# Optimization experiments

Measured on AMD Instinct MI355X. Metric: run time of the kernel, lower is better.

## Reference

```python
import jax, jax.numpy as jnp
import numpy as np

N_BLOCKS, N_LAYERS_PER, RADIX = 4, 10, 2
DILATIONS = [RADIX ** i for i in range(N_LAYERS_PER)] * N_BLOCKS  # 40 layers
NL = len(DILATIONS)
C = 256    # residual_channels
DC = 256   # dilation_channels
SC = 256   # skip_channels
AUX = 80
HOP = 256
CLASSES = 256


def _dilated_causal_conv(x, w, b, d):
    # x: [B, Cin, T], w: [Cout, Cin, K], causal left-pad d*(K-1) (zeropad=True path)
    pad = d * (w.shape[-1] - 1)
    out = jax.lax.conv_general_dilated(
        x, w, window_strides=(1,), padding=[(pad, 0)], rhs_dilation=(d,),
        dimension_numbers=('NCH', 'OIH', 'NCH'))
    return out + b[None, :, None]


def _linear_interp(c, scale):
    # F.interpolate(mode='linear', align_corners=False): out_len = in_len*scale
    Fr = c.shape[-1]
    T = Fr * scale
    pos = jnp.maximum((jnp.arange(T, dtype=jnp.float32) + 0.5) / scale - 0.5, 0.0)
    i0 = jnp.floor(pos).astype(jnp.int32)
    i1 = jnp.minimum(i0 + 1, Fr - 1)
    w = (pos - i0.astype(jnp.float32))
    return c[..., i0] * (1.0 - w) + c[..., i1] * w


def setup_inputs() -> dict:
    key = jax.random.key(0)
    ks = jax.random.split(key, 16)
    B, T, FR = 1, 4096, 16
    s = 0.05
    x = jax.random.randint(ks[0], (B, T), 0, CLASSES)
    y = jax.random.normal(ks[1], (B, AUX, FR), jnp.float32)
    emb_w = jax.random.normal(ks[2], (CLASSES, C), jnp.float32) * s
    emb_w = emb_w.at[CLASSES // 2 - 1].set(0.0)  # padding_idx row is zero
    cond_w = jax.random.normal(ks[3], (2 * DC * NL, AUX), jnp.float32) * s  # 1x1 conv, no bias
    layer_w = jax.random.normal(ks[4], (NL, 2 * DC, C, RADIX), jnp.float32) * s
    layer_b = jax.random.normal(ks[5], (NL, 2 * DC), jnp.float32) * s
    wo_w = jax.random.normal(ks[6], (NL - 1, C + SC, DC), jnp.float32) * s  # res+skip 1x1
    wo_b = jax.random.normal(ks[7], (NL - 1, C + SC), jnp.float32) * s
    last_wo_w = jax.random.normal(ks[8], (SC, DC), jnp.float32) * s         # last layer: skip only
    last_wo_b = jax.random.normal(ks[9], (SC,), jnp.float32) * s
    end1_w = jax.random.normal(ks[10], (SC, SC), jnp.float32) * s
    end1_b = jax.random.normal(ks[11], (SC,), jnp.float32) * s
    end2_w = jax.random.normal(ks[12], (CLASSES, SC), jnp.float32) * s
    end2_b = jax.random.normal(ks[13], (CLASSES,), jnp.float32) * s
    return dict(x=x, y=y, zeropad=1, emb_w=emb_w, cond_w=cond_w,
                layer_w=layer_w, layer_b=layer_b, wo_w=wo_w, wo_b=wo_b,
                last_wo_w=last_wo_w, last_wo_b=last_wo_b,
                end1_w=end1_w, end1_b=end1_b, end2_w=end2_w, end2_b=end2_b)


def reference(x, y, zeropad, emb_w, cond_w, layer_w, layer_b, wo_w, wo_b,
              last_wo_w, last_wo_b, end1_w, end1_b, end2_w, end2_b):
    # embedding + tanh -> [B, C, T]
    h = jnp.tanh(emb_w[x]).transpose(0, 2, 1)
    T = h.shape[-1]
    # conditioner (1x1 conv, no bias) then linear upsample by hop_length
    cond = jnp.einsum('oa,baf->bof', cond_w, y)          # [B, 2*DC*NL, FR]
    cond = _linear_interp(cond, HOP)[..., :T]            # [B, 2*DC*NL, T]
    skip_sum = jnp.zeros((h.shape[0], SC, T), h.dtype)
    for i, d in enumerate(DILATIONS):
        z = _dilated_causal_conv(h, layer_w[i], layer_b[i], d)
        z = z + cond[:, 2 * DC * i:2 * DC * (i + 1)]
        a, g = jnp.split(z, 2, axis=1)
        z = jnp.tanh(a) * jax.nn.sigmoid(g)              # gated activation
        if i < NL - 1:
            o = jnp.einsum('oc,bct->bot', wo_w[i], z) + wo_b[i][None, :, None]
            h = h + o[:, :C]                             # residual
            skip = o[:, C:]
        else:
            skip = jnp.einsum('oc,bct->bot', last_wo_w, z) + last_wo_b[None, :, None]
        skip_sum = skip_sum + skip
    out = jax.nn.relu(skip_sum)
    out = jnp.einsum('oc,bct->bot', end1_w, out) + end1_b[None, :, None]
    out = jax.nn.relu(out)
    out = jnp.einsum('oc,bct->bot', end2_w, out) + end2_b[None, :, None]
    return out  # [B, classes, T]
```

## Files before the change

kernel.cpp:

```cpp
#include <hip/hip_runtime.h>
#include <math.h>

#define T_LEN 4096

typedef __bf16 bf16x8 __attribute__((ext_vector_type(8)));
typedef float  f32x4  __attribute__((ext_vector_type(4)));

union U2 { __bf16 h[2]; unsigned int u; };
union U4 { __bf16 h[4]; uint2 u; };
union U8 { __bf16 h[8]; uint4 u; };

__device__ __forceinline__ void gll16(const void* g, void* l) {
    __builtin_amdgcn_global_load_lds(
        (const __attribute__((address_space(1))) void*)g,
        (__attribute__((address_space(3))) void*)l, 16, 0, 0);
}

__device__ __forceinline__ size_t bfidx(int t, int c) {
    return (size_t)(t >> 4) * 4096 + (size_t)((c >> 5) * 512)
         + (size_t)((((t & 15) + ((c >> 3) & 3) * 16)) * 8) + (c & 7);
}

__global__ __launch_bounds__(256) void embed_kernel(
    const int* __restrict__ x, const float* __restrict__ emb_w,
    float* __restrict__ h, __bf16* __restrict__ XF_hi, __bf16* __restrict__ XF_lo,
    float* __restrict__ skip)
{
    int idx = blockIdx.x * 256 + threadIdx.x;
    int t  = idx & 4095;
    int c2 = (idx >> 12) * 2;
    float2 v = *(const float2*)&emb_w[(size_t)x[t] * 256 + c2];
    float e0 = tanhf(v.x), e1 = tanhf(v.y);
    h[(size_t)c2 * T_LEN + t]       = e0;
    h[(size_t)(c2 + 1) * T_LEN + t] = e1;
    U2 ph, pl;
    ph.h[0] = (__bf16)e0; ph.h[1] = (__bf16)e1;
    pl.h[0] = (__bf16)(e0 - (float)ph.h[0]);
    pl.h[1] = (__bf16)(e1 - (float)ph.h[1]);
    size_t o = bfidx(t, c2);
    *(unsigned int*)(XF_hi + o) = ph.u;
    *(unsigned int*)(XF_lo + o) = pl.u;
    skip[idx * 2]     = 0.0f;
    skip[idx * 2 + 1] = 0.0f;
}

__global__ __launch_bounds__(256) void cond_kernel(
    const float* __restrict__ cond_w, const float* __restrict__ y,
    float* __restrict__ condf)
{
    int idx = blockIdx.x * 256 + threadIdx.x;
    if (idx < 20480 * 16) {
        int o = idx >> 4, f = idx & 15;
        float acc = 0.0f;
        for (int a = 0; a < 80; ++a)
            acc += cond_w[o * 80 + a] * y[a * 16 + f];
        condf[idx] = acc;
    }
}

__global__ __launch_bounds__(256) void skip_cvt_kernel(
    const float* __restrict__ skip,
    __bf16* __restrict__ SF_hi, __bf16* __restrict__ SF_lo)
{
    int idx = blockIdx.x * 256 + threadIdx.x;
    int t  = idx & 4095;
    int c2 = (idx >> 12) * 2;
    float s0 = fmaxf(skip[(size_t)c2 * T_LEN + t], 0.0f);
    float s1 = fmaxf(skip[(size_t)(c2 + 1) * T_LEN + t], 0.0f);
    U2 ph, pl;
    ph.h[0] = (__bf16)s0; ph.h[1] = (__bf16)s1;
    pl.h[0] = (__bf16)(s0 - (float)ph.h[0]);
    pl.h[1] = (__bf16)(s1 - (float)ph.h[1]);
    size_t o = bfidx(t, c2);
    *(unsigned int*)(SF_hi + o) = ph.u;
    *(unsigned int*)(SF_lo + o) = pl.u;
}

__global__ __launch_bounds__(256) void cvt_conv_kernel(
    const float* __restrict__ lw, __bf16* __restrict__ dst)
{
    int f = blockIdx.x * 256 + threadIdx.x;
    int lane = f & 63;
    int mi   = (f >> 6) & 3;
    int kc   = (f >> 8) & 15;
    int gb   = f >> 12;
    int lr = lane & 15, lg = lane >> 4;
    int by = gb & 7, L = gb >> 3;
    int row  = by * 64 + mi * 16 + lr;
    int grow = (row & 1) ? 256 + (row >> 1) : (row >> 1);
    int tap  = (kc >= 8) ? 1 : 0;
    int cb   = (kc & 7) * 32 + lg * 8;
    const float* src = lw + (size_t)L * 262144 + (size_t)grow * 512 + 2 * cb + tap;
    U8 hi, lo;
    #pragma unroll
    for (int j = 0; j < 8; ++j) {
        float v = src[2 * j];
        __bf16 h = (__bf16)v;
        hi.h[j] = h;
        lo.h[j] = (__bf16)(v - (float)h);
    }
    size_t base = (size_t)(gb * 16 + kc) * 4096;
    *(uint4*)(dst + base + (size_t)mi * 512 + lane * 8)        = hi.u;
    *(uint4*)(dst + base + 2048 + (size_t)mi * 512 + lane * 8) = lo.u;
}

__global__ __launch_bounds__(256) void cvt_mat_kernel(
    const float* __restrict__ src, __bf16* __restrict__ dst, int rows)
{
    int f = blockIdx.x * 256 + threadIdx.x;
    if (f >= rows * 32) return;
    int lane = f & 63;
    int mi   = (f >> 6) & 3;
    int kc   = (f >> 8) & 7;
    int by   = f >> 11;
    int L    = blockIdx.y;
    int lr = lane & 15, lg = lane >> 4;
    int row = by * 64 + mi * 16 + lr;
    const float* s = src + (size_t)L * rows * 256 + (size_t)row * 256 + kc * 32 + lg * 8;
    float4 a0 = *(const float4*)(s);
    float4 a1 = *(const float4*)(s + 4);
    float v[8] = {a0.x, a0.y, a0.z, a0.w, a1.x, a1.y, a1.z, a1.w};
    U8 hi, lo;
    #pragma unroll
    for (int j = 0; j < 8; ++j) {
        __bf16 h = (__bf16)v[j];
        hi.h[j] = h;
        lo.h[j] = (__bf16)(v[j] - (float)h);
    }
    size_t base = (size_t)L * rows * 512 + (size_t)(by * 8 + kc) * 4096;
    *(uint4*)(dst + base + (size_t)mi * 512 + lane * 8)        = hi.u;
    *(uint4*)(dst + base + 2048 + (size_t)mi * 512 + lane * 8) = lo.u;
}

template<int MODE>
__global__ __launch_bounds__(256, 2) void gemm_kernel(
    const __bf16* __restrict__ Wpre,
    const __bf16* __restrict__ XF_hi, const __bf16* __restrict__ XF_lo,
    const float*  __restrict__ bias,
    const float*  __restrict__ condL,
    const float*  __restrict__ h_in,
    float*        __restrict__ h_out,
    __bf16*       __restrict__ OF_hi,
    __bf16*       __restrict__ OF_lo,
    float*        __restrict__ skip,
    float*        __restrict__ outp,
    const __bf16* __restrict__ zbuf,
    int d)
{
    constexpr int NK = (MODE == 0) ? 16 : 8;

    __shared__ __bf16 Ab[2][4096];
    __shared__ __bf16 Bb[2][8192];

    const int tid  = threadIdx.x;
    const int t0   = blockIdx.x * 64;
    const int by   = blockIdx.y;
    const int lane = tid & 63;
    const int wid  = tid >> 6;
    const int lg   = lane >> 4;
    const int lr   = lane & 15;
    const int gw   = (t0 >> 4) + wid;

    const __bf16* wbase = Wpre + (size_t)by * NK * 4096;
    const bool smalld = (MODE == 0) && (d < 16);

    f32x4 acc[4];
    #pragma unroll
    for (int mi = 0; mi < 4; ++mi) acc[mi] = (f32x4){0.f, 0.f, 0.f, 0.f};

    auto STAGE = [&](int buf, int kc) {
        const __bf16* ga = wbase + (size_t)kc * 4096 + (wid * 2) * 512 + lane * 8;
        gll16(ga,       &Ab[buf][(wid * 2) * 512]);
        gll16(ga + 512, &Ab[buf][(wid * 2 + 1) * 512]);
        const int kcb = (MODE == 0) ? (kc & 7) : kc;
        if (smalld && kc < 8) {
            const __bf16* h1 = XF_hi + (size_t)gw * 4096 + kcb * 512 + lane * 8;
            const __bf16* l1 = XF_lo + (size_t)gw * 4096 + kcb * 512 + lane * 8;
            const __bf16* h0 = (gw >= 1) ? h1 - 4096 : zbuf + lane * 8;
            const __bf16* l0 = (gw >= 1) ? l1 - 4096 : zbuf + lane * 8;
            gll16(h0, &Bb[buf][(wid * 4 + 0) * 512]);
            gll16(h1, &Bb[buf][(wid * 4 + 1) * 512]);
            gll16(l0, &Bb[buf][(wid * 4 + 2) * 512]);
            gll16(l1, &Bb[buf][(wid * 4 + 3) * 512]);
        } else {
            const int off16 = (MODE == 0 && kc < 8) ? (d >> 4) : 0;
            const int gs = gw - off16;
            const __bf16* sh = (gs >= 0) ? XF_hi + (size_t)gs * 4096 + kcb * 512 + lane * 8
                                         : zbuf + lane * 8;
            const __bf16* sl = (gs >= 0) ? XF_lo + (size_t)gs * 4096 + kcb * 512 + lane * 8
                                         : zbuf + lane * 8;
            gll16(sh, &Bb[buf][(wid * 4 + 0) * 512]);
            gll16(sl, &Bb[buf][(wid * 4 + 2) * 512]);
        }
    };

    STAGE(0, 0);

    for (int kc = 0; kc < NK; ++kc) {
        const int cur = kc & 1;
        if (kc + 1 < NK) {
            STAGE(cur ^ 1, kc + 1);
            asm volatile("s_waitcnt vmcnt(4)" ::: "memory");
        } else {
            asm volatile("s_waitcnt vmcnt(0)" ::: "memory");
        }
        __builtin_amdgcn_sched_barrier(0);
        __builtin_amdgcn_s_barrier();

        bf16x8 Ah[4], Al[4], Bh, Bl;
        #pragma unroll
        for (int mi = 0; mi < 4; ++mi) {
            Ah[mi] = *(const bf16x8*)&Ab[cur][(mi)     * 512 + lane * 8];
            Al[mi] = *(const bf16x8*)&Ab[cur][(4 + mi) * 512 + lane * 8];
        }
        if (smalld && kc < 8) {
            int rr   = lr + 16 - d;
            int q    = wid * 4 + (rr >> 4);
            int slot = (rr & 15) + 16 * lg;
            Bh = *(const bf16x8*)&Bb[cur][q * 512 + slot * 8];
            Bl = *(const bf16x8*)&Bb[cur][(q + 2) * 512 + slot * 8];
        } else {
            Bh = *(const bf16x8*)&Bb[cur][(wid * 4 + 0) * 512 + lane * 8];
            Bl = *(const bf16x8*)&Bb[cur][(wid * 4 + 2) * 512 + lane * 8];
        }
        #pragma unroll
        for (int mi = 0; mi < 4; ++mi) {
            acc[mi] = __builtin_amdgcn_mfma_f32_16x16x32_bf16(Al[mi], Bh, acc[mi], 0, 0, 0);
            acc[mi] = __builtin_amdgcn_mfma_f32_16x16x32_bf16(Ah[mi], Bl, acc[mi], 0, 0, 0);
            acc[mi] = __builtin_amdgcn_mfma_f32_16x16x32_bf16(Ah[mi], Bh, acc[mi], 0, 0, 0);
        }
        asm volatile("s_waitcnt lgkmcnt(0)" ::: "memory");
        __builtin_amdgcn_sched_barrier(0);
        __builtin_amdgcn_s_barrier();
    }

    const int t = t0 + wid * 16 + lr;
    if (MODE == 0) {
        float pos = fmaxf((t + 0.5f) * 0.00390625f - 0.5f, 0.0f);
        int   i0  = (int)pos;
        int   i1  = min(i0 + 1, 15);
        float fw  = pos - (float)i0;
        #pragma unroll
        for (int mi = 0; mi < 4; ++mi) {
            int Rb = by * 64 + mi * 16 + 4 * lg;
            float z[4];
            #pragma unroll
            for (int r = 0; r < 4; ++r) {
                int R  = Rb + r;
                int op = (R & 1) ? 256 + (R >> 1) : (R >> 1);
                const float* cf = condL + op * 16;
                float cv = cf[i0] * (1.0f - fw) + cf[i1] * fw;
                z[r] = acc[mi][r] + bias[op] + cv;
            }
            float u0 = tanhf(z[0]) * (1.0f / (1.0f + expf(-z[1])));
            float u1 = tanhf(z[2]) * (1.0f / (1.0f + expf(-z[3])));
            int cc = Rb >> 1;
            U2 ph, pl;
            ph.h[0] = (__bf16)u0; ph.h[1] = (__bf16)u1;
            pl.h[0] = (__bf16)(u0 - (float)ph.h[0]);
            pl.h[1] = (__bf16)(u1 - (float)ph.h[1]);
            size_t o = bfidx(t, cc);
            *(unsigned int*)(OF_hi + o) = ph.u;
            *(unsigned int*)(OF_lo + o) = pl.u;
        }
    } else if (MODE == 1) {
        #pragma unroll
        for (int mi = 0; mi < 4; ++mi) {
            int Rb = by * 64 + mi * 16 + 4 * lg;
            if (by < 4) {
                U4 ph, pl;
                #pragma unroll
                for (int r = 0; r < 4; ++r) {
                    int R = Rb + r;
                    float o  = acc[mi][r] + bias[R];
                    float nv = h_in[(size_t)R * T_LEN + t] + o;
                    h_out[(size_t)R * T_LEN + t] = nv;
                    __bf16 hi = (__bf16)nv;
                    ph.h[r] = hi;
                    pl.h[r] = (__bf16)(nv - (float)hi);
                }
                size_t o = bfidx(t, Rb);
                *(uint2*)(OF_hi + o) = ph.u;
                *(uint2*)(OF_lo + o) = pl.u;
            } else {
                #pragma unroll
                for (int r = 0; r < 4; ++r) {
                    int R = Rb + r;
                    float* sp = skip + (size_t)(R - 256) * T_LEN + t;
                    *sp += acc[mi][r] + bias[R];
                }
            }
        }
    } else if (MODE == 2) {
        #pragma unroll
        for (int mi = 0; mi < 4; ++mi) {
            int Rb = by * 64 + mi * 16 + 4 * lg;
            #pragma unroll
            for (int r = 0; r < 4; ++r) {
                int R = Rb + r;
                float* sp = skip + (size_t)R * T_LEN + t;
                *sp += acc[mi][r] + bias[R];
            }
        }
    } else if (MODE == 3) {
        #pragma unroll
        for (int mi = 0; mi < 4; ++mi) {
            int Rb = by * 64 + mi * 16 + 4 * lg;
            U4 ph, pl;
            #pragma unroll
            for (int r = 0; r < 4; ++r) {
                int R = Rb + r;
                float m = fmaxf(acc[mi][r] + bias[R], 0.0f);
                __bf16 hi = (__bf16)m;
                ph.h[r] = hi;
                pl.h[r] = (__bf16)(m - (float)hi);
            }
            size_t o = bfidx(t, Rb);
            *(uint2*)(OF_hi + o) = ph.u;
            *(uint2*)(OF_lo + o) = pl.u;
        }
    } else {
        #pragma unroll
        for (int mi = 0; mi < 4; ++mi) {
            int Rb = by * 64 + mi * 16 + 4 * lg;
            #pragma unroll
            for (int r = 0; r < 4; ++r) {
                int R = Rb + r;
                outp[(size_t)R * T_LEN + t] = acc[mi][r] + bias[R];
            }
        }
    }
}

extern "C" void kernel_launch(void* const* d_in, const int* in_sizes, int n_in,
                              void* d_out, int out_size, void* d_ws, size_t ws_size,
                              hipStream_t stream)
{
    const int*   x       = (const int*)  d_in[0];
    const float* y       = (const float*)d_in[1];
    const float* emb_w   = (const float*)d_in[3];
    const float* cond_w  = (const float*)d_in[4];
    const float* layer_w = (const float*)d_in[5];
    const float* layer_b = (const float*)d_in[6];
    const float* wo_w    = (const float*)d_in[7];
    const float* wo_b    = (const float*)d_in[8];
    const float* lwo_w   = (const float*)d_in[9];
    const float* lwo_b   = (const float*)d_in[10];
    const float* e1w     = (const float*)d_in[11];
    const float* e1b     = (const float*)d_in[12];
    const float* e2w     = (const float*)d_in[13];
    const float* e2b     = (const float*)d_in[14];
    float* out = (float*)d_out;

    char* ws = (char*)d_ws;
    const size_t MB = 1024u * 1024u;
    float*  hA     = (float*)(ws);
    float*  hB     = (float*)(ws + 4 * MB);
    float*  skip   = (float*)(ws + 8 * MB);
    float*  condf  = (float*)(ws + 12 * MB);
    __bf16* hFA_hi = (__bf16*)(ws + 14 * MB);
    __bf16* hFA_lo = (__bf16*)(ws + 16 * MB);
    __bf16* hFB_hi = (__bf16*)(ws + 18 * MB);
    __bf16* hFB_lo = (__bf16*)(ws + 20 * MB);
    __bf16* UF_hi  = (__bf16*)(ws + 22 * MB);
    __bf16* UF_lo  = (__bf16*)(ws + 24 * MB);
    __bf16* zbuf   = (__bf16*)(ws + 26 * MB);
    __bf16* convW  = (__bf16*)(ws + 28 * MB);
    __bf16* woW    = (__bf16*)(ws + 68 * MB);
    __bf16* lwoW   = (__bf16*)(ws + 88 * MB);
    __bf16* e1W    = (__bf16*)(ws + 89 * MB);
    __bf16* e2W    = (__bf16*)(ws + 90 * MB);

    hipMemsetAsync(zbuf, 0, 4096, stream);

    cvt_conv_kernel<<<5120, 256, 0, stream>>>(layer_w, convW);
    cvt_mat_kernel<<<dim3(64, 39), 256, 0, stream>>>(wo_w, woW, 512);
    cvt_mat_kernel<<<dim3(32, 1), 256, 0, stream>>>(lwo_w, lwoW, 256);
    cvt_mat_kernel<<<dim3(32, 1), 256, 0, stream>>>(e1w, e1W, 256);
    cvt_mat_kernel<<<dim3(32, 1), 256, 0, stream>>>(e2w, e2W, 256);

    embed_kernel<<<2048, 256, 0, stream>>>(x, emb_w, hA, hFA_hi, hFA_lo, skip);
    cond_kernel<<<(20480 * 16 + 255) / 256, 256, 0, stream>>>(cond_w, y, condf);

    static const int dil[10] = {1, 2, 4, 8, 16, 32, 64, 128, 256, 512};
    float*  hin  = hA;      float*  hout = hB;
    __bf16* hFi_hi = hFA_hi; __bf16* hFi_lo = hFA_lo;
    __bf16* hFo_hi = hFB_hi; __bf16* hFo_lo = hFB_lo;

    for (int i = 0; i < 40; ++i) {
        int d = dil[i % 10];
        const float* lb = layer_b + (size_t)i * 512;
        const float* cL = condf + (size_t)i * 512 * 16;

        gemm_kernel<0><<<dim3(64, 8), 256, 0, stream>>>(
            convW + (size_t)i * 524288, hFi_hi, hFi_lo, lb, cL,
            nullptr, nullptr, UF_hi, UF_lo, nullptr, nullptr, zbuf, d);

        if (i < 39) {
            gemm_kernel<1><<<dim3(64, 8), 256, 0, stream>>>(
                woW + (size_t)i * 262144, UF_hi, UF_lo, wo_b + (size_t)i * 512,
                nullptr, hin, hout, hFo_hi, hFo_lo, skip, nullptr, zbuf, 0);
            float* tf = hin; hin = hout; hout = tf;
            __bf16* t1 = hFi_hi; hFi_hi = hFo_hi; hFo_hi = t1;
            __bf16* t2 = hFi_lo; hFi_lo = hFo_lo; hFo_lo = t2;
        } else {
            gemm_kernel<2><<<dim3(64, 4), 256, 0, stream>>>(
                lwoW, UF_hi, UF_lo, lwo_b,
                nullptr, nullptr, nullptr, nullptr, nullptr, skip, nullptr, zbuf, 0);
        }
    }

    skip_cvt_kernel<<<2048, 256, 0, stream>>>(skip, UF_hi, UF_lo);
    gemm_kernel<3><<<dim3(64, 4), 256, 0, stream>>>(
        e1W, UF_hi, UF_lo, e1b,
        nullptr, nullptr, nullptr, hFA_hi, hFA_lo, nullptr, nullptr, zbuf, 0);
    gemm_kernel<4><<<dim3(64, 4), 256, 0, stream>>>(
        e2W, hFA_hi, hFA_lo, e2b,
        nullptr, nullptr, nullptr, nullptr, nullptr, nullptr, out, zbuf, 0);
}
```

Measured before the change: 1.192 ms.

## Triple-buffer GEMM pipeline, drop fp32 residual, fuse skip ReLU conversion

The GEMM main loop moves from double to triple buffering, with two stages prefetched ahead and raised wave priority around the MFMA block. The small-dilation path becomes a template parameter, so the other variants need less LDS and can run 3 blocks per CU. The fp32 residual copy of h is removed: the residual is rebuilt from the bf16 hi/lo split pair, which cuts global traffic per layer. The skip-to-bf16 conversion with ReLU is fused into the last layer's epilogue, removing one kernel launch.

```diff
diff --git a/kernel.cpp b/kernel.cpp
--- a/kernel.cpp
+++ b/kernel.cpp
@@ -16,6 +16,12 @@
         (__attribute__((address_space(3))) void*)l, 16, 0, 0);
 }
 
+template<int N> __device__ __forceinline__ void vwait() {
+    if constexpr (N == 0)      asm volatile("s_waitcnt vmcnt(0)" ::: "memory");
+    else if constexpr (N == 4) asm volatile("s_waitcnt vmcnt(4)" ::: "memory");
+    else if constexpr (N == 8) asm volatile("s_waitcnt vmcnt(8)" ::: "memory");
+}
+
 __device__ __forceinline__ size_t bfidx(int t, int c) {
     return (size_t)(t >> 4) * 4096 + (size_t)((c >> 5) * 512)
          + (size_t)((((t & 15) + ((c >> 3) & 3) * 16)) * 8) + (c & 7);
@@ -23,7 +29,7 @@
 
 __global__ __launch_bounds__(256) void embed_kernel(
     const int* __restrict__ x, const float* __restrict__ emb_w,
-    float* __restrict__ h, __bf16* __restrict__ XF_hi, __bf16* __restrict__ XF_lo,
+    __bf16* __restrict__ XF_hi, __bf16* __restrict__ XF_lo,
     float* __restrict__ skip)
 {
     int idx = blockIdx.x * 256 + threadIdx.x;
@@ -31,8 +37,6 @@
     int c2 = (idx >> 12) * 2;
     float2 v = *(const float2*)&emb_w[(size_t)x[t] * 256 + c2];
     float e0 = tanhf(v.x), e1 = tanhf(v.y);
-    h[(size_t)c2 * T_LEN + t]       = e0;
-    h[(size_t)(c2 + 1) * T_LEN + t] = e1;
     U2 ph, pl;
     ph.h[0] = (__bf16)e0; ph.h[1] = (__bf16)e1;
     pl.h[0] = (__bf16)(e0 - (float)ph.h[0]);
@@ -56,24 +60,6 @@
             acc += cond_w[o * 80 + a] * y[a * 16 + f];
         condf[idx] = acc;
     }
-}
-
-__global__ __launch_bounds__(256) void skip_cvt_kernel(
-    const float* __restrict__ skip,
-    __bf16* __restrict__ SF_hi, __bf16* __restrict__ SF_lo)
-{
-    int idx = blockIdx.x * 256 + threadIdx.x;
-    int t  = idx & 4095;
-    int c2 = (idx >> 12) * 2;
-    float s0 = fmaxf(skip[(size_t)c2 * T_LEN + t], 0.0f);
-    float s1 = fmaxf(skip[(size_t)(c2 + 1) * T_LEN + t], 0.0f);
-    U2 ph, pl;
-    ph.h[0] = (__bf16)s0; ph.h[1] = (__bf16)s1;
-    pl.h[0] = (__bf16)(s0 - (float)ph.h[0]);
-    pl.h[1] = (__bf16)(s1 - (float)ph.h[1]);
-    size_t o = bfidx(t, c2);
-    *(unsigned int*)(SF_hi + o) = ph.u;
-    *(unsigned int*)(SF_lo + o) = pl.u;
 }
 
 __global__ __launch_bounds__(256) void cvt_conv_kernel(
@@ -132,14 +118,14 @@
     *(uint4*)(dst + base + 2048 + (size_t)mi * 512 + lane * 8) = lo.u;
 }
 
-template<int MODE>
-__global__ __launch_bounds__(256, 2) void gemm_kernel(
+template<int MODE, int SD>
+__global__ __launch_bounds__(256, (MODE == 0 && SD) ? 2 : 3) void gemm_kernel(
     const __bf16* __restrict__ Wpre,
     const __bf16* __restrict__ XF_hi, const __bf16* __restrict__ XF_lo,
     const float*  __restrict__ bias,
     const float*  __restrict__ condL,
-    const float*  __restrict__ h_in,
-    float*        __restrict__ h_out,
+    const __bf16* __restrict__ HFI_hi,
+    const __bf16* __restrict__ HFI_lo,
     __bf16*       __restrict__ OF_hi,
     __bf16*       __restrict__ OF_lo,
     float*        __restrict__ skip,
@@ -147,10 +133,11 @@
     const __bf16* __restrict__ zbuf,
     int d)
 {
-    constexpr int NK = (MODE == 0) ? 16 : 8;
-
-    __shared__ __bf16 Ab[2][4096];
-    __shared__ __bf16 Bb[2][8192];
+    constexpr int NK  = (MODE == 0) ? 16 : 8;
+    constexpr int BCH = (MODE == 0 && SD) ? 8192 : 4096;
+
+    __shared__ __bf16 Ab[3][4096];
+    __shared__ __bf16 Bb[3][BCH];
 
     const int tid  = threadIdx.x;
     const int t0   = blockIdx.x * 64;
@@ -162,7 +149,6 @@
     const int gw   = (t0 >> 4) + wid;
 
     const __bf16* wbase = Wpre + (size_t)by * NK * 4096;
-    const bool smalld = (MODE == 0) && (d < 16);
 
     f32x4 acc[4];
     #pragma unroll
@@ -173,15 +159,22 @@
         gll16(ga,       &Ab[buf][(wid * 2) * 512]);
         gll16(ga + 512, &Ab[buf][(wid * 2 + 1) * 512]);
         const int kcb = (MODE == 0) ? (kc & 7) : kc;
-        if (smalld && kc < 8) {
-            const __bf16* h1 = XF_hi + (size_t)gw * 4096 + kcb * 512 + lane * 8;
-            const __bf16* l1 = XF_lo + (size_t)gw * 4096 + kcb * 512 + lane * 8;
-            const __bf16* h0 = (gw >= 1) ? h1 - 4096 : zbuf + lane * 8;
-            const __bf16* l0 = (gw >= 1) ? l1 - 4096 : zbuf + lane * 8;
-            gll16(h0, &Bb[buf][(wid * 4 + 0) * 512]);
-            gll16(h1, &Bb[buf][(wid * 4 + 1) * 512]);
-            gll16(l0, &Bb[buf][(wid * 4 + 2) * 512]);
-            gll16(l1, &Bb[buf][(wid * 4 + 3) * 512]);
+        if constexpr (MODE == 0 && SD) {
+            if (kc < 8) {
+                const __bf16* h1 = XF_hi + (size_t)gw * 4096 + kcb * 512 + lane * 8;
+                const __bf16* l1 = XF_lo + (size_t)gw * 4096 + kcb * 512 + lane * 8;
+                const __bf16* h0 = (gw >= 1) ? h1 - 4096 : zbuf + lane * 8;
+                const __bf16* l0 = (gw >= 1) ? l1 - 4096 : zbuf + lane * 8;
+                gll16(h0, &Bb[buf][(wid * 4 + 0) * 512]);
+                gll16(h1, &Bb[buf][(wid * 4 + 1) * 512]);
+                gll16(l0, &Bb[buf][(wid * 4 + 2) * 512]);
+                gll16(l1, &Bb[buf][(wid * 4 + 3) * 512]);
+            } else {
+                const __bf16* sh = XF_hi + (size_t)gw * 4096 + kcb * 512 + lane * 8;
+                const __bf16* sl = XF_lo + (size_t)gw * 4096 + kcb * 512 + lane * 8;
+                gll16(sh, &Bb[buf][(wid * 4 + 0) * 512]);
+                gll16(sl, &Bb[buf][(wid * 4 + 2) * 512]);
+            }
         } else {
             const int off16 = (MODE == 0 && kc < 8) ? (d >> 4) : 0;
             const int gs = gw - off16;
@@ -189,21 +182,20 @@
                                          : zbuf + lane * 8;
             const __bf16* sl = (gs >= 0) ? XF_lo + (size_t)gs * 4096 + kcb * 512 + lane * 8
                                          : zbuf + lane * 8;
-            gll16(sh, &Bb[buf][(wid * 4 + 0) * 512]);
-            gll16(sl, &Bb[buf][(wid * 4 + 2) * 512]);
+            gll16(sh, &Bb[buf][(wid * 2) * 512]);
+            gll16(sl, &Bb[buf][(wid * 2 + 1) * 512]);
         }
     };
 
     STAGE(0, 0);
-
+    STAGE(1, 1);
+
+    int cur = 0;
     for (int kc = 0; kc < NK; ++kc) {
-        const int cur = kc & 1;
-        if (kc + 1 < NK) {
-            STAGE(cur ^ 1, kc + 1);
-            asm volatile("s_waitcnt vmcnt(4)" ::: "memory");
-        } else {
-            asm volatile("s_waitcnt vmcnt(0)" ::: "memory");
-        }
+        int pre = cur + 2; if (pre >= 3) pre -= 3;
+        if (kc + 2 < NK)      { STAGE(pre, kc + 2); vwait<8>(); }
+        else if (kc + 1 < NK) { vwait<4>(); }
+        else                  { vwait<0>(); }
         __builtin_amdgcn_sched_barrier(0);
         __builtin_amdgcn_s_barrier();
 
@@ -213,25 +205,33 @@
             Ah[mi] = *(const bf16x8*)&Ab[cur][(mi)     * 512 + lane * 8];
             Al[mi] = *(const bf16x8*)&Ab[cur][(4 + mi) * 512 + lane * 8];
         }
-        if (smalld && kc < 8) {
-            int rr   = lr + 16 - d;
-            int q    = wid * 4 + (rr >> 4);
-            int slot = (rr & 15) + 16 * lg;
-            Bh = *(const bf16x8*)&Bb[cur][q * 512 + slot * 8];
-            Bl = *(const bf16x8*)&Bb[cur][(q + 2) * 512 + slot * 8];
+        if constexpr (MODE == 0 && SD) {
+            if (kc < 8) {
+                int rr   = lr + 16 - d;
+                int q    = wid * 4 + (rr >> 4);
+                int slot = (rr & 15) + 16 * lg;
+                Bh = *(const bf16x8*)&Bb[cur][q * 512 + slot * 8];
+                Bl = *(const bf16x8*)&Bb[cur][(q + 2) * 512 + slot * 8];
+            } else {
+                Bh = *(const bf16x8*)&Bb[cur][(wid * 4 + 0) * 512 + lane * 8];
+                Bl = *(const bf16x8*)&Bb[cur][(wid * 4 + 2) * 512 + lane * 8];
+            }
         } else {
-            Bh = *(const bf16x8*)&Bb[cur][(wid * 4 + 0) * 512 + lane * 8];
-            Bl = *(const bf16x8*)&Bb[cur][(wid * 4 + 2) * 512 + lane * 8];
-        }
+            Bh = *(const bf16x8*)&Bb[cur][(wid * 2) * 512 + lane * 8];
+            Bl = *(const bf16x8*)&Bb[cur][(wid * 2 + 1) * 512 + lane * 8];
+        }
+        __builtin_amdgcn_s_setprio(1);
         #pragma unroll
         for (int mi = 0; mi < 4; ++mi) {
             acc[mi] = __builtin_amdgcn_mfma_f32_16x16x32_bf16(Al[mi], Bh, acc[mi], 0, 0, 0);
             acc[mi] = __builtin_amdgcn_mfma_f32_16x16x32_bf16(Ah[mi], Bl, acc[mi], 0, 0, 0);
             acc[mi] = __builtin_amdgcn_mfma_f32_16x16x32_bf16(Ah[mi], Bh, acc[mi], 0, 0, 0);
         }
+        __builtin_amdgcn_s_setprio(0);
         asm volatile("s_waitcnt lgkmcnt(0)" ::: "memory");
         __builtin_amdgcn_sched_barrier(0);
         __builtin_amdgcn_s_barrier();
+        ++cur; if (cur == 3) cur = 0;
     }
 
     const int t = t0 + wid * 16 + lr;
@@ -268,18 +268,20 @@
         for (int mi = 0; mi < 4; ++mi) {
             int Rb = by * 64 + mi * 16 + 4 * lg;
             if (by < 4) {
+                size_t o = bfidx(t, Rb);
+                U4 hin, lin;
+                hin.u = *(const uint2*)(HFI_hi + o);
+                lin.u = *(const uint2*)(HFI_lo + o);
                 U4 ph, pl;
                 #pragma unroll
                 for (int r = 0; r < 4; ++r) {
                     int R = Rb + r;
-                    float o  = acc[mi][r] + bias[R];
-                    float nv = h_in[(size_t)R * T_LEN + t] + o;
-                    h_out[(size_t)R * T_LEN + t] = nv;
+                    float hv = (float)hin.h[r] + (float)lin.h[r];
+                    float nv = hv + acc[mi][r] + bias[R];
                     __bf16 hi = (__bf16)nv;
                     ph.h[r] = hi;
                     pl.h[r] = (__bf16)(nv - (float)hi);
                 }
-                size_t o = bfidx(t, Rb);
                 *(uint2*)(OF_hi + o) = ph.u;
                 *(uint2*)(OF_lo + o) = pl.u;
             } else {
@@ -295,12 +297,19 @@
         #pragma unroll
         for (int mi = 0; mi < 4; ++mi) {
             int Rb = by * 64 + mi * 16 + 4 * lg;
+            U4 ph, pl;
             #pragma unroll
             for (int r = 0; r < 4; ++r) {
                 int R = Rb + r;
-                float* sp = skip + (size_t)R * T_LEN + t;
-                *sp += acc[mi][r] + bias[R];
-            }
+                float sv = skip[(size_t)R * T_LEN + t] + acc[mi][r] + bias[R];
+                float m  = fmaxf(sv, 0.0f);
+                __bf16 hi = (__bf16)m;
+                ph.h[r] = hi;
+                pl.h[r] = (__bf16)(m - (float)hi);
+            }
+            size_t o = bfidx(t, Rb);
+            *(uint2*)(OF_hi + o) = ph.u;
+            *(uint2*)(OF_lo + o) = pl.u;
         }
     } else if (MODE == 3) {
         #pragma unroll
@@ -354,22 +363,20 @@
 
     char* ws = (char*)d_ws;
     const size_t MB = 1024u * 1024u;
-    float*  hA     = (float*)(ws);
-    float*  hB     = (float*)(ws + 4 * MB);
-    float*  skip   = (float*)(ws + 8 * MB);
-    float*  condf  = (float*)(ws + 12 * MB);
-    __bf16* hFA_hi = (__bf16*)(ws + 14 * MB);
-    __bf16* hFA_lo = (__bf16*)(ws + 16 * MB);
-    __bf16* hFB_hi = (__bf16*)(ws + 18 * MB);
-    __bf16* hFB_lo = (__bf16*)(ws + 20 * MB);
-    __bf16* UF_hi  = (__bf16*)(ws + 22 * MB);
-    __bf16* UF_lo  = (__bf16*)(ws + 24 * MB);
-    __bf16* zbuf   = (__bf16*)(ws + 26 * MB);
-    __bf16* convW  = (__bf16*)(ws + 28 * MB);
-    __bf16* woW    = (__bf16*)(ws + 68 * MB);
-    __bf16* lwoW   = (__bf16*)(ws + 88 * MB);
-    __bf16* e1W    = (__bf16*)(ws + 89 * MB);
-    __bf16* e2W    = (__bf16*)(ws + 90 * MB);
+    float*  skip   = (float*)(ws);
+    float*  condf  = (float*)(ws + 4 * MB);
+    __bf16* hFA_hi = (__bf16*)(ws + 6 * MB);
+    __bf16* hFA_lo = (__bf16*)(ws + 8 * MB);
+    __bf16* hFB_hi = (__bf16*)(ws + 10 * MB);
+    __bf16* hFB_lo = (__bf16*)(ws + 12 * MB);
+    __bf16* UF_hi  = (__bf16*)(ws + 14 * MB);
+    __bf16* UF_lo  = (__bf16*)(ws + 16 * MB);
+    __bf16* zbuf   = (__bf16*)(ws + 18 * MB);
+    __bf16* convW  = (__bf16*)(ws + 20 * MB);
+    __bf16* woW    = (__bf16*)(ws + 60 * MB);
+    __bf16* lwoW   = (__bf16*)(ws + 80 * MB);
+    __bf16* e1W    = (__bf16*)(ws + 81 * MB);
+    __bf16* e2W    = (__bf16*)(ws + 82 * MB);
 
     hipMemsetAsync(zbuf, 0, 4096, stream);
 
@@ -379,11 +386,10 @@
     cvt_mat_kernel<<<dim3(32, 1), 256, 0, stream>>>(e1w, e1W, 256);
     cvt_mat_kernel<<<dim3(32, 1), 256, 0, stream>>>(e2w, e2W, 256);
 
-    embed_kernel<<<2048, 256, 0, stream>>>(x, emb_w, hA, hFA_hi, hFA_lo, skip);
+    embed_kernel<<<2048, 256, 0, stream>>>(x, emb_w, hFA_hi, hFA_lo, skip);
     cond_kernel<<<(20480 * 16 + 255) / 256, 256, 0, stream>>>(cond_w, y, condf);
 
     static const int dil[10] = {1, 2, 4, 8, 16, 32, 64, 128, 256, 512};
-    float*  hin  = hA;      float*  hout = hB;
     __bf16* hFi_hi = hFA_hi; __bf16* hFi_lo = hFA_lo;
     __bf16* hFo_hi = hFB_hi; __bf16* hFo_lo = hFB_lo;
 
@@ -391,30 +397,34 @@
         int d = dil[i % 10];
         const float* lb = layer_b + (size_t)i * 512;
         const float* cL = condf + (size_t)i * 512 * 16;
-
-        gemm_kernel<0><<<dim3(64, 8), 256, 0, stream>>>(
-            convW + (size_t)i * 524288, hFi_hi, hFi_lo, lb, cL,
-            nullptr, nullptr, UF_hi, UF_lo, nullptr, nullptr, zbuf, d);
+        const __bf16* cw = convW + (size_t)i * 524288;
+
+        if (d < 16)
+            gemm_kernel<0, 1><<<dim3(64, 8), 256, 0, stream>>>(
+                cw, hFi_hi, hFi_lo, lb, cL, nullptr, nullptr,
+                UF_hi, UF_lo, nullptr, nullptr, zbuf, d);
+        else
+            gemm_kernel<0, 0><<<dim3(64, 8), 256, 0, stream>>>(
+                cw, hFi_hi, hFi_lo, lb, cL, nullptr, nullptr,
+                UF_hi, UF_lo, nullptr, nullptr, zbuf, d);
 
         if (i < 39) {
-            gemm_kernel<1><<<dim3(64, 8), 256, 0, stream>>>(
+            gemm_kernel<1, 0><<<dim3(64, 8), 256, 0, stream>>>(
                 woW + (size_t)i * 262144, UF_hi, UF_lo, wo_b + (size_t)i * 512,
-                nullptr, hin, hout, hFo_hi, hFo_lo, skip, nullptr, zbuf, 0);
-            float* tf = hin; hin = hout; hout = tf;
+                nullptr, hFi_hi, hFi_lo, hFo_hi, hFo_lo, skip, nullptr, zbuf, 0);
             __bf16* t1 = hFi_hi; hFi_hi = hFo_hi; hFo_hi = t1;
             __bf16* t2 = hFi_lo; hFi_lo = hFo_lo; hFo_lo = t2;
         } else {
-            gemm_kernel<2><<<dim3(64, 4), 256, 0, stream>>>(
+            gemm_kernel<2, 0><<<dim3(64, 4), 256, 0, stream>>>(
                 lwoW, UF_hi, UF_lo, lwo_b,
-                nullptr, nullptr, nullptr, nullptr, nullptr, skip, nullptr, zbuf, 0);
-        }
-    }
-
-    skip_cvt_kernel<<<2048, 256, 0, stream>>>(skip, UF_hi, UF_lo);
-    gemm_kernel<3><<<dim3(64, 4), 256, 0, stream>>>(
-        e1W, UF_hi, UF_lo, e1b,
-        nullptr, nullptr, nullptr, hFA_hi, hFA_lo, nullptr, nullptr, zbuf, 0);
-    gemm_kernel<4><<<dim3(64, 4), 256, 0, stream>>>(
-        e2W, hFA_hi, hFA_lo, e2b,
+                nullptr, nullptr, nullptr, hFo_hi, hFo_lo, skip, nullptr, zbuf, 0);
+        }
+    }
+
+    gemm_kernel<3, 0><<<dim3(64, 4), 256, 0, stream>>>(
+        e1W, hFo_hi, hFo_lo, e1b,
+        nullptr, nullptr, nullptr, UF_hi, UF_lo, nullptr, nullptr, zbuf, 0);
+    gemm_kernel<4, 0><<<dim3(64, 4), 256, 0, stream>>>(
+        e2W, UF_hi, UF_lo, e2b,
         nullptr, nullptr, nullptr, nullptr, nullptr, nullptr, out, zbuf, 0);
 }
```

Result: faster. 1.082 ms (-9.2%).
